# Kernel tuning notes

Measured on AMD Instinct MI355X. Metric: run time of the kernel, lower is better.

The kernel has to match this reference:

```python
import jax, jax.numpy as jnp
import numpy as np

B, N, DIM, H, DH = 2, 2048, 1024, 16, 64  # batch, seq, model dim, heads, head dim
DI = H * DH  # dim_inner = 1024


def setup_inputs() -> dict:
    key = jax.random.key(0)
    kx, km, kq, kkv, ko = jax.random.split(key, 5)
    x = jax.random.normal(kx, (B, N, DIM), dtype=jnp.float32)
    mask = jax.random.randint(km, (B, N), 0, 2).astype(bool)
    mask = mask.at[:, 0].set(True)  # ensure at least one valid key per row
    s = 0.02
    Wq = jax.random.normal(kq, (DIM, DI), dtype=jnp.float32) * s
    Wkv = jax.random.normal(kkv, (DIM, 2 * DI), dtype=jnp.float32) * s
    Wo = jax.random.normal(ko, (DI, DIM), dtype=jnp.float32) * s
    return {"x": x, "mask": mask, "Wq": Wq, "Wkv": Wkv, "Wo": Wo}


def reference(x, mask, Wq, Wkv, Wo):
    scale = DH ** -0.5
    q = x @ Wq                      # [b, n, h*d]
    kv = x @ Wkv                    # [b, n, 2*h*d]  (context = x, self-attention)
    k, v = jnp.split(kv, 2, axis=-1)

    def to_heads(t):
        return t.reshape(B, N, H, DH).transpose(0, 2, 1, 3)  # [b, h, n, d]

    q, k, v = map(to_heads, (q, k, v))
    sim = jnp.einsum('bhid,bhjd->bhij', q, k) * scale        # [b, h, n, n]
    neg = -jnp.finfo(sim.dtype).max
    sim = jnp.where(mask[:, None, None, :], sim, neg)
    attn = jax.nn.softmax(sim, axis=-1)
    out = jnp.einsum('bhij,bhjd->bhid', attn, v)             # [b, h, n, d]
    out = out.transpose(0, 2, 1, 3).reshape(B, N, DI)        # [b, n, h*d]
    return out @ Wo                                          # [b, n, dim]
```

## Files before the change

kernel.cpp:

```cpp
#include <hip/hip_runtime.h>
#include <stdint.h>

typedef __attribute__((ext_vector_type(4))) float f32x4;
typedef __attribute__((ext_vector_type(8))) short s16x8;
typedef __attribute__((ext_vector_type(4))) short s16x4;


__device__ __forceinline__ short f2bf(float f) {
  union { float f; unsigned u; } v; v.f = f;
  unsigned r = (v.u + 0x7fff + ((v.u >> 16) & 1)) >> 16;
  return (short)r;
}

__device__ __forceinline__ unsigned cvtpk(float lo, float hi) {
  unsigned r;
  asm("v_cvt_pk_bf16_f32 %0, %1, %2" : "=v"(r) : "v"(lo), "v"(hi));
  return r;
}

__device__ __forceinline__ void gload16(const void* g, void* l) {
  __builtin_amdgcn_global_load_lds(
      (const __attribute__((address_space(1))) unsigned int*)g,
      (__attribute__((address_space(3))) unsigned int*)l, 16, 0, 0);
}

__global__ __launch_bounds__(256) void cvt_f32_bf16(const float* __restrict__ in,
                                                    short* __restrict__ out, int n4) {
  int i = blockIdx.x * 256 + threadIdx.x;
  if (i >= n4) return;
  float4 f = ((const float4*)in)[i];
  s16x4 o; o.x = f2bf(f.x); o.y = f2bf(f.y); o.z = f2bf(f.z); o.w = f2bf(f.w);
  ((s16x4*)out)[i] = o;
}

__global__ void transpose_cvt3(const float* __restrict__ Wq, const float* __restrict__ Wkv,
                               const float* __restrict__ Wo, short* __restrict__ W1T,
                               short* __restrict__ WoT, float qscale) {
  int bid = blockIdx.x;
  const float* in; short* out; int N; float scale;
  if (bid < 1024)      { in = Wq;  out = W1T;              N = 1024; scale = qscale; }
  else if (bid < 3072) { bid -= 1024; in = Wkv; out = W1T + 1024*1024; N = 2048; scale = 1.f; }
  else                 { bid -= 3072; in = Wo;  out = WoT;             N = 1024; scale = 1.f; }
  const int nb = N >> 5;
  const int nt = (bid % nb) * 32, kt = (bid / nb) * 32;
  __shared__ float t[32][33];
  int tx = threadIdx.x, ty = threadIdx.y;
  #pragma unroll
  for (int i = 0; i < 4; i++) t[ty + 8*i][tx] = in[(size_t)(kt + ty + 8*i) * N + nt + tx];
  __syncthreads();
  #pragma unroll
  for (int i = 0; i < 4; i++)
    out[(size_t)(nt + ty + 8*i) * 1024 + kt + tx] = f2bf(t[tx][ty + 8*i] * scale);
}

__global__ __launch_bounds__(256) void gemm_qkv(const short* __restrict__ A,
                                                const short* __restrict__ Bt,
                                                short* __restrict__ QKV,
                                                short* __restrict__ VT) {
  const int K = 1024;
  __shared__ short As[2][128][32];
  __shared__ short Bs[2][128][32];
  const int tid = threadIdx.x;
  const int wave = tid >> 6, lane = tid & 63;
  const int l15 = lane & 15, l4 = lane >> 4;
  const int bm = blockIdx.y * 128, bn = blockIdx.x * 128;
  const int wr = (wave >> 1) * 64, wc = (wave & 1) * 64;
  const int r = tid >> 2, c8 = (tid & 3) * 8;
  const short* aS0 = &A [(size_t)(bm + r)      * K + c8];
  const short* aS1 = &A [(size_t)(bm + 64 + r) * K + c8];
  const short* bS0 = &Bt[(size_t)(bn + r)      * K + c8];
  const short* bS1 = &Bt[(size_t)(bn + 64 + r) * K + c8];
  f32x4 acc[4][4] = {};
  gload16(aS0, (char*)As + tid*16);
  gload16(aS1, (char*)As + 4096 + tid*16);
  gload16(bS0, (char*)Bs + tid*16);
  gload16(bS1, (char*)Bs + 4096 + tid*16);
  __syncthreads();
  #pragma unroll 2
  for (int kk = 0; kk < 32; kk++) {
    const int cur = kk & 1;
    if (kk + 1 < 32) {
      const int k1 = (kk + 1) * 32;
      gload16(aS0 + k1, (char*)As + (cur^1)*8192 + tid*16);
      gload16(aS1 + k1, (char*)As + (cur^1)*8192 + 4096 + tid*16);
      gload16(bS0 + k1, (char*)Bs + (cur^1)*8192 + tid*16);
      gload16(bS1 + k1, (char*)Bs + (cur^1)*8192 + 4096 + tid*16);
    }
    s16x8 af[4], bf[4];
    #pragma unroll
    for (int m = 0; m < 4; m++) af[m] = *(const s16x8*)&As[cur][wr + m*16 + l15][l4*8];
    #pragma unroll
    for (int n = 0; n < 4; n++) bf[n] = *(const s16x8*)&Bs[cur][wc + n*16 + l15][l4*8];
    #pragma unroll
    for (int m = 0; m < 4; m++)
      #pragma unroll
      for (int n = 0; n < 4; n++)
        acc[m][n] = __builtin_amdgcn_mfma_f32_16x16x32_bf16(af[m], bf[n], acc[m][n], 0, 0, 0);
    __syncthreads();
  }
  #pragma unroll
  for (int m = 0; m < 4; m++)
    #pragma unroll
    for (int n = 0; n < 4; n++) {
      const int row0 = bm + wr + m*16 + l4*4;
      const int col  = bn + wc + n*16 + l15;
      if (col < 2048) {
        #pragma unroll
        for (int j = 0; j < 4; j++)
          QKV[(size_t)(row0 + j) * 3072 + col] = f2bf(acc[m][n][j]);
      } else {
        const int c2 = col - 2048;
        const size_t vtIdx = ((size_t)((row0 >> 11) * 1024 + c2)) * 2048 + (row0 & 2047);
        uint2 pk2;
        pk2.x = cvtpk(acc[m][n][0], acc[m][n][1]);
        pk2.y = cvtpk(acc[m][n][2], acc[m][n][3]);
        *(uint2*)&VT[vtIdx] = pk2;
      }
    }
}

__global__ __launch_bounds__(256) void gemm_out(const short* __restrict__ A,
                                                const short* __restrict__ Bt,
                                                float* __restrict__ C) {
  const int N = 1024, K = 1024;
  __shared__ short As[2][64][32];
  __shared__ short Bs[2][128][32];
  const int tid = threadIdx.x;
  const int wave = tid >> 6, lane = tid & 63;
  const int l15 = lane & 15, l4 = lane >> 4;
  const int bm = blockIdx.y * 64, bn = blockIdx.x * 128;
  const int wr = (wave >> 1) * 32, wc = (wave & 1) * 64;
  const int r = tid >> 2, c8 = (tid & 3) * 8;
  const short* aS0 = &A [(size_t)(bm + r)      * K + c8];
  const short* bS0 = &Bt[(size_t)(bn + r)      * K + c8];
  const short* bS1 = &Bt[(size_t)(bn + 64 + r) * K + c8];
  f32x4 acc[2][4] = {};
  if (r < 64) gload16(aS0, (char*)As + tid*16);
  gload16(bS0, (char*)Bs + tid*16);
  gload16(bS1, (char*)Bs + 4096 + tid*16);
  __syncthreads();
  #pragma unroll 2
  for (int kk = 0; kk < 32; kk++) {
    const int cur = kk & 1;
    if (kk + 1 < 32) {
      const int k1 = (kk + 1) * 32;
      gload16(aS0 + k1, (char*)As + (cur^1)*4096 + tid*16);
      gload16(bS0 + k1, (char*)Bs + (cur^1)*8192 + tid*16);
      gload16(bS1 + k1, (char*)Bs + (cur^1)*8192 + 4096 + tid*16);
    }
    s16x8 af[2], bf[4];
    #pragma unroll
    for (int m = 0; m < 2; m++) af[m] = *(const s16x8*)&As[cur][wr + m*16 + l15][l4*8];
    #pragma unroll
    for (int n = 0; n < 4; n++) bf[n] = *(const s16x8*)&Bs[cur][wc + n*16 + l15][l4*8];
    #pragma unroll
    for (int m = 0; m < 2; m++)
      #pragma unroll
      for (int n = 0; n < 4; n++)
        acc[m][n] = __builtin_amdgcn_mfma_f32_16x16x32_bf16(af[m], bf[n], acc[m][n], 0, 0, 0);
    __syncthreads();
  }
  #pragma unroll
  for (int m = 0; m < 2; m++)
    #pragma unroll
    for (int n = 0; n < 4; n++)
      #pragma unroll
      for (int j = 0; j < 4; j++) {
        int row = bm + wr + m*16 + l4*4 + j;
        int col = bn + wc + n*16 + l15;
        C[(size_t)row * N + col] = acc[m][n][j];
      }
}

__global__ __launch_bounds__(256) void attn_kernel(const short* __restrict__ QKV,
                                                   const short* __restrict__ VT,
                                                   const int* __restrict__ mask,
                                                   short* __restrict__ O) {
  __shared__ float biasLds[2048];
  __shared__ short Ks[2][64*64];
  __shared__ short Vs[2][64*64];
  __shared__ short Pl[4][32*64];

  const int orig = blockIdx.y * 16 + blockIdx.x;
  const int wg = (orig & 7) * 64 + (orig >> 3);
  const int qt = wg & 15;
  const int bh = wg >> 4;
  const int b = bh >> 4, h = bh & 15;
  const int tid = threadIdx.x;
  const int wave = tid >> 6, lane = tid & 63;
  const int l15 = lane & 15, l4 = lane >> 4;

  const int q0 = qt * 128 + wave * 32;
  s16x8 qb[2][2];
  #pragma unroll
  for (int qg = 0; qg < 2; qg++)
    #pragma unroll
    for (int s = 0; s < 2; s++)
      qb[qg][s] = *(const s16x8*)&QKV[(size_t)(b*2048 + q0 + qg*16 + l15) * 3072 + h*64 + s*32 + l4*8];

  for (int j = tid; j < 2048; j += 256)
    biasLds[j] = mask[b*2048 + j] ? 0.0f : -1e38f;

  const int r0 = tid >> 3, c0 = tid & 7;
  const int cs = (c0 ^ (r0 & 7)) * 8;
  const short* Kg = QKV + (size_t)(b*2048)*3072 + 1024 + h*64;
  const short* Vg = VT + (size_t)(bh*64)*2048;
  const short* kS0 = Kg + (size_t)r0*3072 + cs;
  const short* kS1 = Kg + (size_t)(r0+32)*3072 + cs;
  const short* vS0 = Vg + (size_t)r0*2048 + cs;
  const short* vS1 = Vg + (size_t)(r0+32)*2048 + cs;

  gload16(kS0, (char*)Ks[0] + tid*16);
  gload16(kS1, (char*)Ks[0] + 4096 + tid*16);
  gload16(vS0, (char*)Vs[0] + tid*16);
  gload16(vS1, (char*)Vs[0] + 4096 + tid*16);
  __syncthreads();

  f32x4 oacc[2][4] = {};
  float mrun[2] = {12.0f, 12.0f}, lsum[2] = {0.0f, 0.0f};
  const int swz = (l15 & 7) << 4;
  char* PlB = (char*)&Pl[wave][0];

  #pragma unroll 2
  for (int kt = 0; kt < 32; kt++) {
    const int cur = kt & 1;
    if (kt + 1 < 32) {
      gload16(kS0 + (size_t)(kt+1)*196608, (char*)Ks[cur^1] + tid*16);
      gload16(kS1 + (size_t)(kt+1)*196608, (char*)Ks[cur^1] + 4096 + tid*16);
      gload16(vS0 + (kt+1)*64,             (char*)Vs[cur^1] + tid*16);
      gload16(vS1 + (kt+1)*64,             (char*)Vs[cur^1] + 4096 + tid*16);
    }
    const char* KsB = (const char*)Ks[cur];
    const char* VsB = (const char*)Vs[cur];

    s16x8 ka[4][2];
    #pragma unroll
    for (int g = 0; g < 4; g++) {
      ka[g][0] = *(const s16x8*)(KsB + (g*16 + l15)*128 + ((l4*16) ^ swz));
      ka[g][1] = *(const s16x8*)(KsB + (g*16 + l15)*128 + ((64 + l4*16) ^ swz));
    }
    f32x4 sv[2][4];
    #pragma unroll
    for (int g = 0; g < 4; g++) {
      f32x4 cb = *(const f32x4*)&biasLds[kt*64 + g*16 + l4*4];
      #pragma unroll
      for (int qg = 0; qg < 2; qg++) {
        f32x4 s = __builtin_amdgcn_mfma_f32_16x16x32_bf16(ka[g][0], qb[qg][0], cb, 0, 0, 0);
        sv[qg][g] = __builtin_amdgcn_mfma_f32_16x16x32_bf16(ka[g][1], qb[qg][1], s, 0, 0, 0);
      }
    }

    #pragma unroll
    for (int qg = 0; qg < 2; qg++) {
      const int rowB = (qg*16 + l15) * 128;
      float p[16], psum = 0.f;
      #pragma unroll
      for (int g = 0; g < 4; g++)
        #pragma unroll
        for (int rr = 0; rr < 4; rr++) {
          p[g*4+rr] = __builtin_amdgcn_exp2f(sv[qg][g][rr] - mrun[qg]);
          psum += p[g*4+rr];
        }
      psum += __shfl_xor(psum, 16);
      psum += __shfl_xor(psum, 32);
      if (!__all(psum <= 512.0f)) {
        float tm = sv[qg][0][0];
        #pragma unroll
        for (int g = 0; g < 4; g++)
          #pragma unroll
          for (int rr = 0; rr < 4; rr++) tm = fmaxf(tm, sv[qg][g][rr]);
        tm = fmaxf(tm, __shfl_xor(tm, 16));
        tm = fmaxf(tm, __shfl_xor(tm, 32));
        float mnew = fmaxf(mrun[qg], tm);
        float corr = __builtin_amdgcn_exp2f(mrun[qg] - mnew);
        psum = 0.f;
        #pragma unroll
        for (int g = 0; g < 4; g++)
          #pragma unroll
          for (int rr = 0; rr < 4; rr++) {
            p[g*4+rr] = __builtin_amdgcn_exp2f(sv[qg][g][rr] - mnew);
            psum += p[g*4+rr];
          }
        psum += __shfl_xor(psum, 16);
        psum += __shfl_xor(psum, 32);
        #pragma unroll
        for (int f = 0; f < 4; f++)
          #pragma unroll
          for (int j = 0; j < 4; j++) oacc[qg][f][j] *= corr;
        lsum[qg] *= corr;
        mrun[qg] = mnew;
      }
      lsum[qg] += psum;
      #pragma unroll
      for (int g = 0; g < 4; g++) {
        uint2 pk2;
        pk2.x = cvtpk(p[g*4+0], p[g*4+1]);
        pk2.y = cvtpk(p[g*4+2], p[g*4+3]);
        *(uint2*)(PlB + rowB + ((g*32 + l4*8) ^ swz)) = pk2;
      }
      #pragma unroll
      for (int kh = 0; kh < 2; kh++) {
        s16x8 pb = *(const s16x8*)(PlB + rowB + ((kh*64 + l4*16) ^ swz));
        #pragma unroll
        for (int f = 0; f < 4; f++) {
          s16x8 vf = *(const s16x8*)(VsB + (f*16 + l15)*128 + ((kh*64 + l4*16) ^ swz));
          oacc[qg][f] = __builtin_amdgcn_mfma_f32_16x16x32_bf16(vf, pb, oacc[qg][f], 0, 0, 0);
        }
      }
    }
    __syncthreads();
  }

  #pragma unroll
  for (int qg = 0; qg < 2; qg++) {
    float inv = 1.0f / lsum[qg];
    #pragma unroll
    for (int f = 0; f < 4; f++) {
      uint2 o;
      o.x = cvtpk(oacc[qg][f][0] * inv, oacc[qg][f][1] * inv);
      o.y = cvtpk(oacc[qg][f][2] * inv, oacc[qg][f][3] * inv);
      *(uint2*)&O[(size_t)(b*2048 + q0 + qg*16 + l15) * 1024 + h*64 + f*16 + l4*4] = o;
    }
  }
}

extern "C" void kernel_launch(void* const* d_in, const int* in_sizes, int n_in,
                              void* d_out, int out_size, void* d_ws, size_t ws_size,
                              hipStream_t stream) {
  const float* x    = (const float*)d_in[0];
  const int*   mask = (const int*)  d_in[1];
  const float* Wq   = (const float*)d_in[2];
  const float* Wkv  = (const float*)d_in[3];
  const float* Wo   = (const float*)d_in[4];
  float* out = (float*)d_out;

  char* ws = (char*)d_ws;
  short* xb  = (short*)(ws);
  short* W1T = (short*)(ws + 8388608);
  short* WoT = (short*)(ws + 14680064);
  short* QKV = (short*)(ws + 16777216);
  short* VT  = (short*)(ws + 41943040);
  short* O   = (short*)(ws + 50331648);

  const float qscale = 0.18033688011112042f;

  cvt_f32_bf16<<<4096, 256, 0, stream>>>(x, xb, 4194304 / 4);
  transpose_cvt3<<<4096, dim3(32, 8), 0, stream>>>(Wq, Wkv, Wo, W1T, WoT, qscale);
  gemm_qkv<<<dim3(24, 32), 256, 0, stream>>>(xb, W1T, QKV, VT);
  attn_kernel<<<dim3(16, 32), 256, 0, stream>>>(QKV, VT, mask, O);
  gemm_out<<<dim3(8, 64), 256, 0, stream>>>(O, WoT, out);
}
```

Baseline: 208.8 us.

## Compact unmasked keys/values so attention iterates only over valid key tiles

A prefix scan over the key mask gives each valid key a compacted position. The QKV GEMM epilogue scatters K and V rows to those positions, and the padding up to a multiple of 64 is zero-filled. Attention then loops only over ceil(nv/64) key tiles and applies the bias only on the last tile, so roughly half the masked key work is skipped for random masks. The conversion, transpose and scan kernels are merged into one prep launch. The cost is that V is now written as scalar scattered stores instead of packed ones, plus a serial single-thread scan per batch.

New measurement: 209.5 us. Within noise of the previous version (+0.4%).

```diff
diff --git a/kernel.cpp b/kernel.cpp
--- a/kernel.cpp
+++ b/kernel.cpp
@@ -24,39 +24,77 @@
       (__attribute__((address_space(3))) unsigned int*)l, 16, 0, 0);
 }
 
-__global__ __launch_bounds__(256) void cvt_f32_bf16(const float* __restrict__ in,
-                                                    short* __restrict__ out, int n4) {
-  int i = blockIdx.x * 256 + threadIdx.x;
-  if (i >= n4) return;
-  float4 f = ((const float4*)in)[i];
-  s16x4 o; o.x = f2bf(f.x); o.y = f2bf(f.y); o.z = f2bf(f.z); o.w = f2bf(f.w);
-  ((s16x4*)out)[i] = o;
-}
-
-__global__ void transpose_cvt3(const float* __restrict__ Wq, const float* __restrict__ Wkv,
-                               const float* __restrict__ Wo, short* __restrict__ W1T,
-                               short* __restrict__ WoT, float qscale) {
+__global__ __launch_bounds__(256) void prep(const float* __restrict__ x, short* __restrict__ xb,
+                                            const float* __restrict__ Wq, const float* __restrict__ Wkv,
+                                            const float* __restrict__ Wo, short* __restrict__ W1T,
+                                            short* __restrict__ WoT, float qscale,
+                                            const int* __restrict__ mask, int* __restrict__ pos,
+                                            int* __restrict__ nvOut, short* __restrict__ QK,
+                                            short* __restrict__ VT) {
+  __shared__ float tbuf[32][33];
+  __shared__ int part[256];
+  __shared__ int nvLds;
   int bid = blockIdx.x;
-  const float* in; short* out; int N; float scale;
-  if (bid < 1024)      { in = Wq;  out = W1T;              N = 1024; scale = qscale; }
-  else if (bid < 3072) { bid -= 1024; in = Wkv; out = W1T + 1024*1024; N = 2048; scale = 1.f; }
-  else                 { bid -= 3072; in = Wo;  out = WoT;             N = 1024; scale = 1.f; }
-  const int nb = N >> 5;
-  const int nt = (bid % nb) * 32, kt = (bid / nb) * 32;
-  __shared__ float t[32][33];
-  int tx = threadIdx.x, ty = threadIdx.y;
-  #pragma unroll
-  for (int i = 0; i < 4; i++) t[ty + 8*i][tx] = in[(size_t)(kt + ty + 8*i) * N + nt + tx];
+  const int tid = threadIdx.x;
+
+  if (bid < 4096) {
+    int i = bid * 256 + tid;
+    float4 f = ((const float4*)x)[i];
+    s16x4 o; o.x = f2bf(f.x); o.y = f2bf(f.y); o.z = f2bf(f.z); o.w = f2bf(f.w);
+    ((s16x4*)xb)[i] = o;
+    return;
+  }
+  bid -= 4096;
+  if (bid < 4096) {
+    const float* in; short* out; int N; float scale;
+    if (bid < 1024)      { in = Wq;  out = W1T;              N = 1024; scale = qscale; }
+    else if (bid < 3072) { bid -= 1024; in = Wkv; out = W1T + 1024*1024; N = 2048; scale = 1.f; }
+    else                 { bid -= 3072; in = Wo;  out = WoT;             N = 1024; scale = 1.f; }
+    const int nb = N >> 5;
+    const int nt = (bid % nb) * 32, kt = (bid / nb) * 32;
+    const int tx = tid & 31, ty = tid >> 5;
+    #pragma unroll
+    for (int i = 0; i < 4; i++) tbuf[ty + 8*i][tx] = in[(size_t)(kt + ty + 8*i) * N + nt + tx];
+    __syncthreads();
+    #pragma unroll
+    for (int i = 0; i < 4; i++)
+      out[(size_t)(nt + ty + 8*i) * 1024 + kt + tx] = f2bf(tbuf[tx][ty + 8*i] * scale);
+    return;
+  }
+  const int b = bid - 4096;
+  int loc[8], s = 0;
+  #pragma unroll
+  for (int j = 0; j < 8; j++) { loc[j] = mask[b*2048 + tid*8 + j] ? 1 : 0; s += loc[j]; }
+  part[tid] = s;
   __syncthreads();
-  #pragma unroll
-  for (int i = 0; i < 4; i++)
-    out[(size_t)(nt + ty + 8*i) * 1024 + kt + tx] = f2bf(t[tx][ty + 8*i] * scale);
+  if (tid == 0) {
+    int run = 0;
+    for (int i = 0; i < 256; i++) { int v = part[i]; part[i] = run; run += v; }
+    nvOut[b] = run; nvLds = run;
+  }
+  __syncthreads();
+  int run = part[tid];
+  #pragma unroll
+  for (int j = 0; j < 8; j++) { pos[b*2048 + tid*8 + j] = loc[j] ? run : -1; run += loc[j]; }
+  const int nv = nvLds;
+  const int padded = (nv + 63) & ~63;
+  const int w = padded - nv;
+  s16x8 z8 = {0,0,0,0,0,0,0,0};
+  for (int idx = tid; idx < w * 128; idx += 256) {
+    int rr = idx >> 7, cc = idx & 127;
+    *(s16x8*)&QK[((size_t)(b*2048 + nv + rr)) * 2048 + 1024 + cc*8] = z8;
+  }
+  for (int idx = tid; idx < 1024 * w; idx += 256) {
+    int dr = idx / w, col = nv + idx % w;
+    VT[((size_t)(b*1024 + dr)) * 2048 + col] = 0;
+  }
 }
 
 __global__ __launch_bounds__(256) void gemm_qkv(const short* __restrict__ A,
                                                 const short* __restrict__ Bt,
-                                                short* __restrict__ QKV,
-                                                short* __restrict__ VT) {
+                                                short* __restrict__ QK,
+                                                short* __restrict__ VT,
+                                                const int* __restrict__ pos) {
   const int K = 1024;
   __shared__ short As[2][128][32];
   __shared__ short Bs[2][128][32];
@@ -99,24 +137,32 @@
     __syncthreads();
   }
   #pragma unroll
-  for (int m = 0; m < 4; m++)
+  for (int m = 0; m < 4; m++) {
+    const int row0 = bm + wr + m*16 + l4*4;
+    const int b2 = row0 >> 11;
+    int4 p4 = *(const int4*)&pos[row0];
+    const int pj[4] = {p4.x, p4.y, p4.z, p4.w};
     #pragma unroll
     for (int n = 0; n < 4; n++) {
-      const int row0 = bm + wr + m*16 + l4*4;
-      const int col  = bn + wc + n*16 + l15;
-      if (col < 2048) {
+      const int col = bn + wc + n*16 + l15;
+      if (col < 1024) {
         #pragma unroll
         for (int j = 0; j < 4; j++)
-          QKV[(size_t)(row0 + j) * 3072 + col] = f2bf(acc[m][n][j]);
+          QK[(size_t)(row0 + j) * 2048 + col] = f2bf(acc[m][n][j]);
+      } else if (col < 2048) {
+        #pragma unroll
+        for (int j = 0; j < 4; j++)
+          if (pj[j] >= 0)
+            QK[((size_t)(b2*2048 + pj[j])) * 2048 + col] = f2bf(acc[m][n][j]);
       } else {
         const int c2 = col - 2048;
-        const size_t vtIdx = ((size_t)((row0 >> 11) * 1024 + c2)) * 2048 + (row0 & 2047);
-        uint2 pk2;
-        pk2.x = cvtpk(acc[m][n][0], acc[m][n][1]);
-        pk2.y = cvtpk(acc[m][n][2], acc[m][n][3]);
-        *(uint2*)&VT[vtIdx] = pk2;
-      }
-    }
+        const size_t base = ((size_t)(b2*1024 + c2)) * 2048;
+        #pragma unroll
+        for (int j = 0; j < 4; j++)
+          if (pj[j] >= 0) VT[base + pj[j]] = f2bf(acc[m][n][j]);
+      }
+    }
+  }
 }
 
 __global__ __launch_bounds__(256) void gemm_out(const short* __restrict__ A,
@@ -172,11 +218,10 @@
       }
 }
 
-__global__ __launch_bounds__(256) void attn_kernel(const short* __restrict__ QKV,
+__global__ __launch_bounds__(256) void attn_kernel(const short* __restrict__ QK,
                                                    const short* __restrict__ VT,
-                                                   const int* __restrict__ mask,
+                                                   const int* __restrict__ nv,
                                                    short* __restrict__ O) {
-  __shared__ float biasLds[2048];
   __shared__ short Ks[2][64*64];
   __shared__ short Vs[2][64*64];
   __shared__ short Pl[4][32*64];
@@ -190,23 +235,23 @@
   const int wave = tid >> 6, lane = tid & 63;
   const int l15 = lane & 15, l4 = lane >> 4;
 
+  const int nvb = nv[b];
+  const int nt = (nvb + 63) >> 6;
+
   const int q0 = qt * 128 + wave * 32;
   s16x8 qb[2][2];
   #pragma unroll
   for (int qg = 0; qg < 2; qg++)
     #pragma unroll
     for (int s = 0; s < 2; s++)
-      qb[qg][s] = *(const s16x8*)&QKV[(size_t)(b*2048 + q0 + qg*16 + l15) * 3072 + h*64 + s*32 + l4*8];
-
-  for (int j = tid; j < 2048; j += 256)
-    biasLds[j] = mask[b*2048 + j] ? 0.0f : -1e38f;
+      qb[qg][s] = *(const s16x8*)&QK[(size_t)(b*2048 + q0 + qg*16 + l15) * 2048 + h*64 + s*32 + l4*8];
 
   const int r0 = tid >> 3, c0 = tid & 7;
   const int cs = (c0 ^ (r0 & 7)) * 8;
-  const short* Kg = QKV + (size_t)(b*2048)*3072 + 1024 + h*64;
+  const short* Kg = QK + (size_t)(b*2048)*2048 + 1024 + h*64;
   const short* Vg = VT + (size_t)(bh*64)*2048;
-  const short* kS0 = Kg + (size_t)r0*3072 + cs;
-  const short* kS1 = Kg + (size_t)(r0+32)*3072 + cs;
+  const short* kS0 = Kg + (size_t)r0*2048 + cs;
+  const short* kS1 = Kg + (size_t)(r0+32)*2048 + cs;
   const short* vS0 = Vg + (size_t)r0*2048 + cs;
   const short* vS1 = Vg + (size_t)(r0+32)*2048 + cs;
 
@@ -218,20 +263,22 @@
 
   f32x4 oacc[2][4] = {};
   float mrun[2] = {12.0f, 12.0f}, lsum[2] = {0.0f, 0.0f};
+  const f32x4 zf = {0.f, 0.f, 0.f, 0.f};
   const int swz = (l15 & 7) << 4;
   char* PlB = (char*)&Pl[wave][0];
 
   #pragma unroll 2
-  for (int kt = 0; kt < 32; kt++) {
+  for (int kt = 0; kt < nt; kt++) {
     const int cur = kt & 1;
-    if (kt + 1 < 32) {
-      gload16(kS0 + (size_t)(kt+1)*196608, (char*)Ks[cur^1] + tid*16);
-      gload16(kS1 + (size_t)(kt+1)*196608, (char*)Ks[cur^1] + 4096 + tid*16);
+    if (kt + 1 < nt) {
+      gload16(kS0 + (size_t)(kt+1)*131072, (char*)Ks[cur^1] + tid*16);
+      gload16(kS1 + (size_t)(kt+1)*131072, (char*)Ks[cur^1] + 4096 + tid*16);
       gload16(vS0 + (kt+1)*64,             (char*)Vs[cur^1] + tid*16);
       gload16(vS1 + (kt+1)*64,             (char*)Vs[cur^1] + 4096 + tid*16);
     }
     const char* KsB = (const char*)Ks[cur];
     const char* VsB = (const char*)Vs[cur];
+    const bool last = (kt == nt - 1);
 
     s16x8 ka[4][2];
     #pragma unroll
@@ -242,7 +289,12 @@
     f32x4 sv[2][4];
     #pragma unroll
     for (int g = 0; g < 4; g++) {
-      f32x4 cb = *(const f32x4*)&biasLds[kt*64 + g*16 + l4*4];
+      f32x4 cb = zf;
+      if (last) {
+        const int k0i = kt*64 + g*16 + l4*4;
+        #pragma unroll
+        for (int rr = 0; rr < 4; rr++) cb[rr] = (k0i + rr < nvb) ? 0.f : -1e38f;
+      }
       #pragma unroll
       for (int qg = 0; qg < 2; qg++) {
         f32x4 s = __builtin_amdgcn_mfma_f32_16x16x32_bf16(ka[g][0], qb[qg][0], cb, 0, 0, 0);
@@ -338,15 +390,16 @@
   short* xb  = (short*)(ws);
   short* W1T = (short*)(ws + 8388608);
   short* WoT = (short*)(ws + 14680064);
-  short* QKV = (short*)(ws + 16777216);
-  short* VT  = (short*)(ws + 41943040);
-  short* O   = (short*)(ws + 50331648);
+  short* QK  = (short*)(ws + 16777216);
+  short* VT  = (short*)(ws + 33554432);
+  short* O   = (short*)(ws + 41943040);
+  int*   pos = (int*)  (ws + 50331648);
+  int*   nvP = (int*)  (ws + 50348032);
 
   const float qscale = 0.18033688011112042f;
 
-  cvt_f32_bf16<<<4096, 256, 0, stream>>>(x, xb, 4194304 / 4);
-  transpose_cvt3<<<4096, dim3(32, 8), 0, stream>>>(Wq, Wkv, Wo, W1T, WoT, qscale);
-  gemm_qkv<<<dim3(24, 32), 256, 0, stream>>>(xb, W1T, QKV, VT);
-  attn_kernel<<<dim3(16, 32), 256, 0, stream>>>(QKV, VT, mask, O);
+  prep<<<8194, 256, 0, stream>>>(x, xb, Wq, Wkv, Wo, W1T, WoT, qscale, mask, pos, nvP, QK, VT);
+  gemm_qkv<<<dim3(24, 32), 256, 0, stream>>>(xb, W1T, QK, VT, pos);
+  attn_kernel<<<dim3(16, 32), 256, 0, stream>>>(QK, VT, nvP, O);
   gemm_out<<<dim3(8, 64), 256, 0, stream>>>(O, WoT, out);
 }
```
